# Performance work log

Hardware: AMD Instinct MI355X
Metric: run time of the kernel (lower is better)

Reference implementation:

```python
import jax, jax.numpy as jnp
import numpy as np

B, N, OBS, HID, H = 8, 1024, 64, 192, 3
D = HID // H  # head_dim = 64
ALPHA = 0.2   # LeakyReLU negative slope
NEG = -9e15   # mask value from torch code (-9000000000000000.0)


def gat_layer(h, adj, W, a):
    """Multi-head GAT layer, math-identical to the torch per-head loop.
    h: (B,N,F_in), adj: (N,N), W: (H,F_in,D), a: (H,2D).
    Concat-score a^T [Wh_i || Wh_j] is split into a_l^T Wh_i + a_r^T Wh_j
    (broadcast-add) to avoid materializing the N^2 x 2D tensor.
    """
    Wh = jnp.einsum('bni,hid->bhnd', h, W)           # (B,H,N,D)
    d = Wh.shape[-1]
    s_i = jnp.einsum('bhnd,hd->bhn', Wh, a[:, :d])   # a_l . Wh_i
    s_j = jnp.einsum('bhnd,hd->bhn', Wh, a[:, d:])   # a_r . Wh_j
    e = s_i[..., :, None] + s_j[..., None, :]        # (B,H,N,N)
    e = jnp.where(e > 0, e, ALPHA * e)               # LeakyReLU
    e = jnp.where(adj > 0, e, NEG)                   # adjacency mask
    attn = jax.nn.softmax(e, axis=-1)                # (dropout=0 in eval)
    out = jnp.einsum('bhnm,bhmd->bhnd', attn, Wh)    # weighted aggregate
    b, nh, n, _ = out.shape
    return out.transpose(0, 2, 1, 3).reshape(b, n, nh * d)  # concat heads


def setup_inputs() -> dict:
    key = jax.random.key(0)
    k1, k2, k3, k4, k5 = jax.random.split(key, 5)
    h = jax.random.normal(k1, (B, N, OBS), dtype=jnp.float32)
    adj = jnp.ones((N, N), dtype=jnp.float32)  # graph_type='full'
    # xavier_uniform-style scale (gain=1.414)
    def xav(k, shape, fan_in, fan_out):
        lim = 1.414 * np.sqrt(6.0 / (fan_in + fan_out))
        return jax.random.uniform(k, shape, jnp.float32, -lim, lim)
    W1 = xav(k2, (H, OBS, D), OBS, D)
    a1 = xav(k3, (H, 2 * D), 2 * D, 1)
    W2 = xav(k4, (H, HID, D), HID, D)
    a2 = xav(k5, (H, 2 * D), 2 * D, 1)
    return {"h": h, "adj": adj, "W1": W1, "a1": a1, "W2": W2, "a2": a2}


def reference(h, adj, W1, a1, W2, a2):
    x = gat_layer(h, adj, W1, a1)   # (B,N,HID)
    x = jax.nn.elu(x)               # inter-layer nonlinearity
    x = gat_layer(x, adj, W2, a2)   # (B,N,HID)
    return x
```

## Files before the change

### kernel.cpp

```cpp
#include <hip/hip_runtime.h>
#include <math.h>

#define Bc   8
#define Nc   1024
#define OBSc 64
#define HIDc 192
#define NHc  3
#define Dc   64
#define ALPHAc 0.2f

typedef __attribute__((ext_vector_type(8))) _Float16 half8;
typedef __attribute__((ext_vector_type(4))) float floatx4;


__global__ __launch_bounds__(256) void k_proj1(
    const float* __restrict__ xin, const float* __restrict__ W1,
    const float* __restrict__ a1, _Float16* __restrict__ WhT,
    float* __restrict__ si, float* __restrict__ sj, float* __restrict__ Mp1,
    const float* __restrict__ adj, unsigned long long* __restrict__ adjb,
    const float* __restrict__ W2, _Float16* __restrict__ W2T)
{
    const int tid = threadIdx.x;
    const int bh  = blockIdx.y;

    if (bh == Bc * NHc) {
        const int px = blockIdx.x, wv = tid >> 6, lane = tid & 63;
        for (int r8 = 0; r8 < 8; ++r8) {
            const int i = px * 32 + wv * 8 + r8;
            unsigned long long word = 0;
            for (int g = 0; g < 16; ++g) {
                bool c = adj[(size_t)i * Nc + g * 64 + lane] > 0.f;
                unsigned long long bal = __ballot(c);
                if (lane == g) word = bal;
            }
            if (lane < 16) adjb[(size_t)i * 16 + lane] = word;
        }
        if (px < 12) {
            for (int e = px * 3072 + tid; e < px * 3072 + 3072; e += 256) {
                int t = e & 7, ln = (e >> 3) & 63, p = (e >> 9) & 1, nh = (e >> 10) & 1;
                int g = e >> 11; int ks = g % 6, hh = g / 6;
                int k = ks * 32 + (ln >> 4) * 8 + t;
                int d = nh * 32 + p * 16 + (ln & 15);
                W2T[e] = (_Float16)W2[((size_t)hh * HIDc + k) * Dc + d];
            }
        }
        return;
    }

    __shared__ union {
        _Float16 Bs[64][OBSc + 8];
        _Float16 Ts[64][40];
    } u;
    __shared__ float spsAi[32], spsAj[32], spsBi[32], spsBj[32];

    const int b = bh / NHc, hh = bh % NHc;
    const int row0 = blockIdx.x * 32;

    for (int e = tid; e < OBSc * 64; e += 256) {
        int k = e >> 6, d = e & 63;
        u.Bs[d][k] = (_Float16)W1[(size_t)hh * OBSc * 64 + e];
    }
    __syncthreads();

    const int lane = tid & 63, wv = tid >> 6;
    const int mblk = (wv & 1) * 16, nhalf = (wv >> 1) * 32;
    const int fr = lane & 15, fq = lane >> 4;
    floatx4 acc0 = {0.f,0.f,0.f,0.f}, acc1 = {0.f,0.f,0.f,0.f};
    const int row = row0 + mblk + fr;

#pragma unroll
    for (int ks = 0; ks < OBSc / 32; ++ks) {
        const int k0 = ks * 32 + fq * 8;
        const float* xr = xin + ((size_t)b * Nc + row) * OBSc + k0;
        float4 u0 = *(const float4*)xr;
        float4 u1 = *(const float4*)(xr + 4);
        half8 af;
        af[0] = (_Float16)u0.x; af[1] = (_Float16)u0.y;
        af[2] = (_Float16)u0.z; af[3] = (_Float16)u0.w;
        af[4] = (_Float16)u1.x; af[5] = (_Float16)u1.y;
        af[6] = (_Float16)u1.z; af[7] = (_Float16)u1.w;
        half8 b0 = *(const half8*)&u.Bs[nhalf + fr][k0];
        half8 b1 = *(const half8*)&u.Bs[nhalf + 16 + fr][k0];
        acc0 = __builtin_amdgcn_mfma_f32_16x16x32_f16(af, b0, acc0, 0, 0, 0);
        acc1 = __builtin_amdgcn_mfma_f32_16x16x32_f16(af, b1, acc1, 0, 0, 0);
    }

    const float al0 = a1[hh * 2 * Dc + nhalf + fr];
    const float al1 = a1[hh * 2 * Dc + nhalf + 16 + fr];
    const float ar0 = a1[hh * 2 * Dc + Dc + nhalf + fr];
    const float ar1 = a1[hh * 2 * Dc + Dc + nhalf + 16 + fr];
    float pi[4], pj[4];
#pragma unroll
    for (int r = 0; r < 4; ++r) {
        pi[r] = acc0[r] * al0 + acc1[r] * al1;
        pj[r] = acc0[r] * ar0 + acc1[r] * ar1;
        for (int off = 8; off >= 1; off >>= 1) {
            pi[r] += __shfl_xor(pi[r], off, 64);
            pj[r] += __shfl_xor(pj[r], off, 64);
        }
    }
    if (fr == 0) {
#pragma unroll
        for (int r = 0; r < 4; ++r) {
            int lr = mblk + fq * 4 + r;
            if (nhalf == 0) { spsAi[lr] = pi[r]; spsAj[lr] = pj[r]; }
            else            { spsBi[lr] = pi[r]; spsBj[lr] = pj[r]; }
        }
    }
    __syncthreads();
    if (tid < 64) {
        float vj = -INFINITY;
        if (tid < 32) {
            size_t g = (size_t)bh * Nc + row0 + tid;
            si[g] = spsAi[tid] + spsBi[tid];
            vj    = spsAj[tid] + spsBj[tid];
            sj[g] = vj;
        }
        float mv = vj;
        for (int off = 32; off >= 1; off >>= 1) mv = fmaxf(mv, __shfl_xor(mv, off, 64));
        if (tid == 0) Mp1[bh * 32 + blockIdx.x] = mv;
    }

#pragma unroll
    for (int nt = 0; nt < 2; ++nt) {
        const int d = nhalf + nt * 16 + fr;
        floatx4 acc = nt ? acc1 : acc0;
#pragma unroll
        for (int p = 0; p < 2; ++p) {
            union { unsigned int w; _Float16 h[2]; } pk;
            pk.h[0] = (_Float16)acc[2 * p];
            pk.h[1] = (_Float16)acc[2 * p + 1];
            *(unsigned int*)&u.Ts[d][mblk + fq * 4 + 2 * p] = pk.w;
        }
    }
    __syncthreads();
    {
        const int c2 = tid >> 6, lane2 = tid & 63;
        const int fr2 = lane2 & 15, fq2 = lane2 >> 4;
        const int jt = row0 >> 5;
        uint4 v = *(const uint4*)&u.Ts[c2 * 16 + fr2][fq2 * 8];
        *(uint4*)&WhT[(size_t)(bh * 32 + jt) * 2048 + tid * 8] = v;
    }
}

__global__ __launch_bounds__(384, 2) void k_fused(
    const _Float16* __restrict__ WhT1,
    const float* __restrict__ si1, const float* __restrict__ sj1,
    const float* __restrict__ Mp1, const unsigned long long* __restrict__ adjb,
    const _Float16* __restrict__ W2T, const float* __restrict__ a2,
    _Float16* __restrict__ WhT2,
    float* __restrict__ si2, float* __restrict__ sj2, float* __restrict__ Mp2)
{
    __shared__ union {
        struct { float red[6][64][20]; float zs[6][16]; } ag;
        _Float16 Ts3[3][64][24];
    } uR;
    __shared__ _Float16 xhs[16][208];
    __shared__ float sp2i[6][16], sp2j[6][16];
    __shared__ float sjs[3][1024];
    __shared__ unsigned long long adjs[16][16];

    const int tid = threadIdx.x, wv = tid >> 6, lane = tid & 63;
    const int b = blockIdx.x >> 6, c16 = blockIdx.x & 63;
    const int row0 = c16 * 16;
    const int hh = wv >> 1, kh = wv & 1;
    const int bh = b * NHc + hh;
    const int fr = lane & 15, fq = lane >> 4;
    const int row = row0 + fr;

    for (int e = tid; e < 768; e += 384) {
        int h = e >> 8, idx = (e & 255) * 4;
        *(float4*)&sjs[h][idx] = *(const float4*)&sj1[(size_t)(b * NHc + h) * Nc + idx];
    }
    if (tid < 256)
        adjs[tid >> 4][tid & 15] = adjb[(size_t)(row0 + (tid >> 4)) * 16 + (tid & 15)];
    __syncthreads();

    float mpv = Mp1[bh * 32 + (lane & 31)];
    for (int off = 16; off >= 1; off >>= 1) mpv = fmaxf(mpv, __shfl_xor(mpv, off, 64));
    const float s_i = si1[(size_t)bh * Nc + row];
    const float em  = s_i + mpv;
    const float m_i = fmaxf(em, ALPHAc * em);

    const _Float16* Bp = WhT1 + (size_t)bh * 65536 + (size_t)kh * 32768 + lane * 8;

    floatx4 acc[4] = {{0.f,0.f,0.f,0.f},{0.f,0.f,0.f,0.f},
                      {0.f,0.f,0.f,0.f},{0.f,0.f,0.f,0.f}};
    float zacc = 0.f;

    half8 bf[3][4];
#pragma unroll
    for (int st = 0; st < 2; ++st)
#pragma unroll
        for (int c = 0; c < 4; ++c)
            bf[st][c] = *(const half8*)(Bp + (size_t)st * 2048 + c * 512);

#pragma unroll
    for (int s16 = 0; s16 < 16; ++s16) {
        const int s   = kh * 16 + s16;
        const int cur = s16 % 3;
        if (s16 < 14) {
            const int nxt = (s16 + 2) % 3;
            const _Float16* bn = Bp + (size_t)(s16 + 2) * 2048;
#pragma unroll
            for (int c = 0; c < 4; ++c)
                bf[nxt][c] = *(const half8*)(bn + c * 512);
        }
        const float4 sa = *(const float4*)&sjs[hh][s * 32 + fq * 8];
        const float4 sb = *(const float4*)&sjs[hh][s * 32 + fq * 8 + 4];
        const unsigned long long w = adjs[fr][s >> 1];
        const int bb = (s & 1) * 32 + fq * 8;
        const float sv[8] = {sa.x, sa.y, sa.z, sa.w, sb.x, sb.y, sb.z, sb.w};
        float p[8];
        if (w == ~0ULL) {
#pragma unroll
            for (int t = 0; t < 8; ++t) {
                float e = s_i + sv[t];
                e = fmaxf(e, ALPHAc * e) - m_i;
                p[t] = __expf(e);
            }
        } else {
#pragma unroll
            for (int t = 0; t < 8; ++t) {
                float e = s_i + sv[t];
                e = fmaxf(e, ALPHAc * e) - m_i;
                e = ((w >> (bb + t)) & 1) ? e : -1e30f;
                p[t] = __expf(e);
            }
        }
        zacc += ((p[0] + p[1]) + (p[2] + p[3])) + ((p[4] + p[5]) + (p[6] + p[7]));
        union { half8 v; _Float16 h[8]; } A;
#pragma unroll
        for (int t = 0; t < 8; ++t) A.h[t] = (_Float16)p[t];
        acc[0] = __builtin_amdgcn_mfma_f32_16x16x32_f16(A.v, bf[cur][0], acc[0], 0, 0, 0);
        acc[1] = __builtin_amdgcn_mfma_f32_16x16x32_f16(A.v, bf[cur][1], acc[1], 0, 0, 0);
        acc[2] = __builtin_amdgcn_mfma_f32_16x16x32_f16(A.v, bf[cur][2], acc[2], 0, 0, 0);
        acc[3] = __builtin_amdgcn_mfma_f32_16x16x32_f16(A.v, bf[cur][3], acc[3], 0, 0, 0);
    }

    zacc += __shfl_xor(zacc, 16, 64);
    zacc += __shfl_xor(zacc, 32, 64);
    if (lane < 16) uR.ag.zs[wv][lane] = zacc;
#pragma unroll
    for (int c = 0; c < 4; ++c)
        *(floatx4*)&uR.ag.red[wv][lane][c * 4] = acc[c];
    __syncthreads();

    {
        const int w0 = hh * 2;
#pragma unroll
        for (int cc = 0; cc < 2; ++cc) {
            const int c = kh * 2 + cc;
#pragma unroll
            for (int reg = 0; reg < 4; ++reg) {
                const int r = fq * 4 + reg;
                const float af = uR.ag.red[w0][lane][c * 4 + reg]
                               + uR.ag.red[w0 + 1][lane][c * 4 + reg];
                const float Z = uR.ag.zs[w0][r] + uR.ag.zs[w0 + 1][r];
                float v = af / Z;
                v = v > 0.f ? v : expm1f(v);
                xhs[r][hh * 64 + c * 16 + fr] = (_Float16)v;
            }
        }
    }
    __syncthreads();

    floatx4 a2c0 = {0.f,0.f,0.f,0.f}, a2c1 = {0.f,0.f,0.f,0.f};
#pragma unroll
    for (int ks = 0; ks < 6; ++ks) {
        half8 af2 = *(const half8*)&xhs[fr][ks * 32 + fq * 8];
        const _Float16* wb = W2T + (size_t)((hh * 6 + ks) * 2 + kh) * 1024 + lane * 8;
        half8 b0 = *(const half8*)wb;
        half8 b1 = *(const half8*)(wb + 512);
        a2c0 = __builtin_amdgcn_mfma_f32_16x16x32_f16(af2, b0, a2c0, 0, 0, 0);
        a2c1 = __builtin_amdgcn_mfma_f32_16x16x32_f16(af2, b1, a2c1, 0, 0, 0);
    }

    {
        const float* a2h = a2 + hh * 2 * Dc;
        const float al0 = a2h[kh * 32 + fr];
        const float al1 = a2h[kh * 32 + 16 + fr];
        const float ar0 = a2h[Dc + kh * 32 + fr];
        const float ar1 = a2h[Dc + kh * 32 + 16 + fr];
#pragma unroll
        for (int reg = 0; reg < 4; ++reg) {
            float pi = a2c0[reg] * al0 + a2c1[reg] * al1;
            float pj = a2c0[reg] * ar0 + a2c1[reg] * ar1;
            for (int off = 8; off >= 1; off >>= 1) {
                pi += __shfl_xor(pi, off, 64);
                pj += __shfl_xor(pj, off, 64);
            }
            if (fr == 0) {
                sp2i[wv][fq * 4 + reg] = pi;
                sp2j[wv][fq * 4 + reg] = pj;
            }
        }
    }
    __syncthreads();

    if (kh == 0 && lane < 16) {
        const int r = lane;
        float vi = sp2i[wv][r] + sp2i[wv + 1][r];
        float vj = sp2j[wv][r] + sp2j[wv + 1][r];
        si2[(size_t)bh * Nc + row0 + r] = vi;
        sj2[(size_t)bh * Nc + row0 + r] = vj;
        float mv = vj;
        for (int off = 8; off >= 1; off >>= 1) mv = fmaxf(mv, __shfl_xor(mv, off, 64));
        if (r == 0) Mp2[bh * 64 + c16] = mv;
    }
#pragma unroll
    for (int cc = 0; cc < 2; ++cc) {
        const int d = kh * 32 + cc * 16 + fr;
        floatx4 av = cc ? a2c1 : a2c0;
#pragma unroll
        for (int p = 0; p < 2; ++p) {
            union { unsigned int w2; _Float16 h[2]; } pk;
            pk.h[0] = (_Float16)av[2 * p];
            pk.h[1] = (_Float16)av[2 * p + 1];
            *(unsigned int*)&uR.Ts3[hh][d][fq * 4 + 2 * p] = pk.w2;
        }
    }
    __syncthreads();

    {
        const int hh3 = tid / 128, rem = tid % 128, d3 = rem >> 1, rr = rem & 1;
        uint4 v = *(const uint4*)&uR.Ts3[hh3][d3][rr * 8];
        const int bh3 = b * NHc + hh3;
        const int jt = c16 >> 1;
        const int c3 = d3 >> 4;
        const int fqp = (c16 & 1) * 2 + rr;
        *(uint4*)&WhT2[((((size_t)(bh3 * 32 + jt) * 4 + c3) * 64) + fqp * 16 + (d3 & 15)) * 8] = v;
    }
}

__global__ __launch_bounds__(256, 4) void k_aggr2(
    const _Float16* __restrict__ WhT,
    const float* __restrict__ si, const float* __restrict__ sj,
    const float* __restrict__ Mp2, const unsigned long long* __restrict__ adjb,
    float* __restrict__ out)
{
    __shared__ float red[4][64][20];
    __shared__ float zs[4][16];
    __shared__ float sjs[1024];
    __shared__ unsigned long long adjs[16][16];

    const int tid  = threadIdx.x;
    const int wv   = tid >> 6, lane = tid & 63;
    const int bh   = blockIdx.x >> 6;
    const int row0 = (blockIdx.x & 63) << 4;
    const int b    = bh / NHc, hh = bh % NHc;
    const int fr   = lane & 15, fq = lane >> 4;
    const int row  = row0 + fr;

    for (int e = tid; e < 256; e += 256)
        *(float4*)&sjs[e * 4] = *(const float4*)&sj[(size_t)bh * Nc + e * 4];
    if (tid < 256 && tid >= 0) {  }
    if (tid < 256)
        adjs[tid >> 4][tid & 15] = adjb[(size_t)(row0 + (tid >> 4)) * 16 + (tid & 15)];
    __syncthreads();

    float mpv = Mp2[bh * 64 + lane];
    for (int off = 32; off >= 1; off >>= 1) mpv = fmaxf(mpv, __shfl_xor(mpv, off, 64));

    const float s_i = si[(size_t)bh * Nc + row];
    const float em  = s_i + mpv;
    const float m_i = fmaxf(em, ALPHAc * em);

    const _Float16* Bp = WhT + (size_t)bh * 65536 + (size_t)wv * 8 * 2048 + lane * 8;

    floatx4 acc[4] = {{0.f,0.f,0.f,0.f},{0.f,0.f,0.f,0.f},
                      {0.f,0.f,0.f,0.f},{0.f,0.f,0.f,0.f}};
    float zacc = 0.f;

    half8 bf[3][4];
#pragma unroll
    for (int st = 0; st < 2; ++st)
#pragma unroll
        for (int c = 0; c < 4; ++c)
            bf[st][c] = *(const half8*)(Bp + (size_t)st * 2048 + c * 512);

#pragma unroll
    for (int s8 = 0; s8 < 8; ++s8) {
        const int s   = wv * 8 + s8;
        const int cur = s8 % 3;
        if (s8 < 6) {
            const int nxt = (s8 + 2) % 3;
            const _Float16* bn = Bp + (size_t)(s8 + 2) * 2048;
#pragma unroll
            for (int c = 0; c < 4; ++c)
                bf[nxt][c] = *(const half8*)(bn + c * 512);
        }
        const float4 sa = *(const float4*)&sjs[s * 32 + fq * 8];
        const float4 sb = *(const float4*)&sjs[s * 32 + fq * 8 + 4];
        const unsigned long long w = adjs[fr][s >> 1];
        const int bb = (s & 1) * 32 + fq * 8;
        const float sv[8] = {sa.x, sa.y, sa.z, sa.w, sb.x, sb.y, sb.z, sb.w};
        float p[8];
        if (w == ~0ULL) {
#pragma unroll
            for (int t = 0; t < 8; ++t) {
                float e = s_i + sv[t];
                e = fmaxf(e, ALPHAc * e) - m_i;
                p[t] = __expf(e);
            }
        } else {
#pragma unroll
            for (int t = 0; t < 8; ++t) {
                float e = s_i + sv[t];
                e = fmaxf(e, ALPHAc * e) - m_i;
                e = ((w >> (bb + t)) & 1) ? e : -1e30f;
                p[t] = __expf(e);
            }
        }
        zacc += ((p[0] + p[1]) + (p[2] + p[3])) + ((p[4] + p[5]) + (p[6] + p[7]));
        union { half8 v; _Float16 h[8]; } A;
#pragma unroll
        for (int t = 0; t < 8; ++t) A.h[t] = (_Float16)p[t];
        acc[0] = __builtin_amdgcn_mfma_f32_16x16x32_f16(A.v, bf[cur][0], acc[0], 0, 0, 0);
        acc[1] = __builtin_amdgcn_mfma_f32_16x16x32_f16(A.v, bf[cur][1], acc[1], 0, 0, 0);
        acc[2] = __builtin_amdgcn_mfma_f32_16x16x32_f16(A.v, bf[cur][2], acc[2], 0, 0, 0);
        acc[3] = __builtin_amdgcn_mfma_f32_16x16x32_f16(A.v, bf[cur][3], acc[3], 0, 0, 0);
    }

    zacc += __shfl_xor(zacc, 16, 64);
    zacc += __shfl_xor(zacc, 32, 64);
    if (lane < 16) zs[wv][lane] = zacc;
#pragma unroll
    for (int c = 0; c < 4; ++c)
        *(floatx4*)&red[wv][lane][c * 4] = acc[c];
    __syncthreads();

    floatx4 af = {0.f, 0.f, 0.f, 0.f};
#pragma unroll
    for (int w2 = 0; w2 < 4; ++w2) {
        floatx4 r = *(const floatx4*)&red[w2][lane][wv * 4];
        af[0] += r[0]; af[1] += r[1]; af[2] += r[2]; af[3] += r[3];
    }
#pragma unroll
    for (int reg = 0; reg < 4; ++reg) {
        const int r = fq * 4 + reg;
        const float Z = (zs[0][r] + zs[1][r]) + (zs[2][r] + zs[3][r]);
        out[((size_t)b * Nc + row0 + r) * HIDc + hh * Dc + wv * 16 + fr] = af[reg] / Z;
    }
}

extern "C" void kernel_launch(void* const* d_in, const int* in_sizes, int n_in,
                              void* d_out, int out_size, void* d_ws, size_t ws_size,
                              hipStream_t stream) {
    const float* h_in = (const float*)d_in[0];
    const float* adj  = (const float*)d_in[1];
    const float* W1   = (const float*)d_in[2];
    const float* a1   = (const float*)d_in[3];
    const float* W2   = (const float*)d_in[4];
    const float* a2   = (const float*)d_in[5];
    float* out = (float*)d_out;

    float* ws = (float*)d_ws;
    const size_t nWhT_f = (size_t)Bc * NHc * Dc * Nc / 2;
    const size_t nAb_f  = (size_t)Nc * 16 * 2;
    const size_t nW2T_f = 36864 / 2;
    const size_t nR     = (size_t)Bc * NHc * Nc;
    _Float16* WhT1 = (_Float16*)ws;
    _Float16* WhT2 = (_Float16*)(ws + nWhT_f);
    unsigned long long* adjb = (unsigned long long*)(ws + 2 * nWhT_f);
    _Float16* W2T  = (_Float16*)(ws + 2 * nWhT_f + nAb_f);
    float* si1 = ws + 2 * nWhT_f + nAb_f + nW2T_f;
    float* sj1 = si1 + nR;
    float* si2 = sj1 + nR;
    float* sj2 = si2 + nR;
    float* Mp1 = sj2 + nR;
    float* Mp2 = Mp1 + 768;

    k_proj1<<<dim3(Nc / 32, Bc * NHc + 1), 256, 0, stream>>>(
        h_in, W1, a1, WhT1, si1, sj1, Mp1, adj, adjb, W2, W2T);

    k_fused<<<512, 384, 0, stream>>>(
        WhT1, si1, sj1, Mp1, adjb, W2T, a2, WhT2, si2, sj2, Mp2);

    k_aggr2<<<1536, 256, 0, stream>>>(WhT2, si2, sj2, Mp2, adjb, out);
}
```

Measured before the change: 117.6 us.

## Enlarge row tiles to 64 and stage Wh tiles through double-buffered LDS

Both attention kernels now process 64 query rows per block instead of 16. Each block streams the full key range through double-buffered shared memory, and waves split rows instead of keys, which removes the cross-wave split-K reduction through LDS. The aim is to reuse each loaded Wh tile across more rows and cut redundant global reads. In exchange, grids shrink to 128 and 384 blocks, which lowers parallelism on a many-CU GPU, and a __syncthreads is added per key step.

Measured after the change: 127.7 us. 1.09x slower.

```diff
diff --git a/kernel.cpp b/kernel.cpp
--- a/kernel.cpp
+++ b/kernel.cpp
@@ -152,184 +152,195 @@
     float* __restrict__ si2, float* __restrict__ sj2, float* __restrict__ Mp2)
 {
     __shared__ union {
-        struct { float red[6][64][20]; float zs[6][16]; } ag;
-        _Float16 Ts3[3][64][24];
-    } uR;
-    __shared__ _Float16 xhs[16][208];
-    __shared__ float sp2i[6][16], sp2j[6][16];
+        _Float16 bufs[2][3][2048];
+        _Float16 Ts3[3][64][72];
+    } u;
+    __shared__ _Float16 xhs[64][216];
     __shared__ float sjs[3][1024];
-    __shared__ unsigned long long adjs[16][16];
+    __shared__ unsigned long long adjs[64][16];
 
     const int tid = threadIdx.x, wv = tid >> 6, lane = tid & 63;
-    const int b = blockIdx.x >> 6, c16 = blockIdx.x & 63;
-    const int row0 = c16 * 16;
-    const int hh = wv >> 1, kh = wv & 1;
+    const int b = blockIdx.x >> 4, c64 = blockIdx.x & 15;
+    const int row0 = c64 * 64;
+    const int hh = wv >> 1, mh = wv & 1;
     const int bh = b * NHc + hh;
     const int fr = lane & 15, fq = lane >> 4;
-    const int row = row0 + fr;
 
     for (int e = tid; e < 768; e += 384) {
         int h = e >> 8, idx = (e & 255) * 4;
         *(float4*)&sjs[h][idx] = *(const float4*)&sj1[(size_t)(b * NHc + h) * Nc + idx];
     }
-    if (tid < 256)
-        adjs[tid >> 4][tid & 15] = adjb[(size_t)(row0 + (tid >> 4)) * 16 + (tid & 15)];
-    __syncthreads();
+    for (int e = tid; e < 1024; e += 384)
+        adjs[e >> 4][e & 15] = adjb[(size_t)(row0 + (e >> 4)) * 16 + (e & 15)];
+
+    const int sh = tid / 128;
+    const int so = (tid & 127) * 8;
+    const _Float16* SBp = WhT1 + (size_t)(b * NHc + sh) * 65536 + so;
+    uint4 st0 = *(const uint4*)(SBp);
+    uint4 st1 = *(const uint4*)(SBp + 1024);
+    *(uint4*)&u.bufs[0][sh][so] = st0;
+    *(uint4*)&u.bufs[0][sh][so + 1024] = st1;
+    st0 = *(const uint4*)(SBp + 2048);
+    st1 = *(const uint4*)(SBp + 2048 + 1024);
 
     float mpv = Mp1[bh * 32 + (lane & 31)];
     for (int off = 16; off >= 1; off >>= 1) mpv = fmaxf(mpv, __shfl_xor(mpv, off, 64));
-    const float s_i = si1[(size_t)bh * Nc + row];
-    const float em  = s_i + mpv;
-    const float m_i = fmaxf(em, ALPHAc * em);
-
-    const _Float16* Bp = WhT1 + (size_t)bh * 65536 + (size_t)kh * 32768 + lane * 8;
-
-    floatx4 acc[4] = {{0.f,0.f,0.f,0.f},{0.f,0.f,0.f,0.f},
-                      {0.f,0.f,0.f,0.f},{0.f,0.f,0.f,0.f}};
-    float zacc = 0.f;
-
-    half8 bf[3][4];
-#pragma unroll
-    for (int st = 0; st < 2; ++st)
-#pragma unroll
-        for (int c = 0; c < 4; ++c)
-            bf[st][c] = *(const half8*)(Bp + (size_t)st * 2048 + c * 512);
-
-#pragma unroll
-    for (int s16 = 0; s16 < 16; ++s16) {
-        const int s   = kh * 16 + s16;
-        const int cur = s16 % 3;
-        if (s16 < 14) {
-            const int nxt = (s16 + 2) % 3;
-            const _Float16* bn = Bp + (size_t)(s16 + 2) * 2048;
-#pragma unroll
-            for (int c = 0; c < 4; ++c)
-                bf[nxt][c] = *(const half8*)(bn + c * 512);
+    float s_i[2], m_i[2];
+#pragma unroll
+    for (int mt = 0; mt < 2; ++mt) {
+        s_i[mt] = si1[(size_t)bh * Nc + row0 + mh * 32 + mt * 16 + fr];
+        float em = s_i[mt] + mpv;
+        m_i[mt] = fmaxf(em, ALPHAc * em);
+    }
+    __syncthreads();
+
+    floatx4 acc[2][4] = {{{0.f,0.f,0.f,0.f},{0.f,0.f,0.f,0.f},{0.f,0.f,0.f,0.f},{0.f,0.f,0.f,0.f}},
+                         {{0.f,0.f,0.f,0.f},{0.f,0.f,0.f,0.f},{0.f,0.f,0.f,0.f},{0.f,0.f,0.f,0.f}}};
+    float zacc[2] = {0.f, 0.f};
+
+#pragma unroll 2
+    for (int s = 0; s < 32; ++s) {
+        const int cur = s & 1;
+        if (s < 31) {
+            *(uint4*)&u.bufs[cur ^ 1][sh][so] = st0;
+            *(uint4*)&u.bufs[cur ^ 1][sh][so + 1024] = st1;
+            if (s < 30) {
+                st0 = *(const uint4*)(SBp + (size_t)(s + 2) * 2048);
+                st1 = *(const uint4*)(SBp + (size_t)(s + 2) * 2048 + 1024);
+            }
         }
         const float4 sa = *(const float4*)&sjs[hh][s * 32 + fq * 8];
         const float4 sb = *(const float4*)&sjs[hh][s * 32 + fq * 8 + 4];
-        const unsigned long long w = adjs[fr][s >> 1];
+        const float sv[8] = {sa.x, sa.y, sa.z, sa.w, sb.x, sb.y, sb.z, sb.w};
         const int bb = (s & 1) * 32 + fq * 8;
-        const float sv[8] = {sa.x, sa.y, sa.z, sa.w, sb.x, sb.y, sb.z, sb.w};
-        float p[8];
-        if (w == ~0ULL) {
-#pragma unroll
-            for (int t = 0; t < 8; ++t) {
-                float e = s_i + sv[t];
-                e = fmaxf(e, ALPHAc * e) - m_i;
-                p[t] = __expf(e);
-            }
-        } else {
-#pragma unroll
-            for (int t = 0; t < 8; ++t) {
-                float e = s_i + sv[t];
-                e = fmaxf(e, ALPHAc * e) - m_i;
-                e = ((w >> (bb + t)) & 1) ? e : -1e30f;
-                p[t] = __expf(e);
-            }
-        }
-        zacc += ((p[0] + p[1]) + (p[2] + p[3])) + ((p[4] + p[5]) + (p[6] + p[7]));
-        union { half8 v; _Float16 h[8]; } A;
-#pragma unroll
-        for (int t = 0; t < 8; ++t) A.h[t] = (_Float16)p[t];
-        acc[0] = __builtin_amdgcn_mfma_f32_16x16x32_f16(A.v, bf[cur][0], acc[0], 0, 0, 0);
-        acc[1] = __builtin_amdgcn_mfma_f32_16x16x32_f16(A.v, bf[cur][1], acc[1], 0, 0, 0);
-        acc[2] = __builtin_amdgcn_mfma_f32_16x16x32_f16(A.v, bf[cur][2], acc[2], 0, 0, 0);
-        acc[3] = __builtin_amdgcn_mfma_f32_16x16x32_f16(A.v, bf[cur][3], acc[3], 0, 0, 0);
-    }
-
-    zacc += __shfl_xor(zacc, 16, 64);
-    zacc += __shfl_xor(zacc, 32, 64);
-    if (lane < 16) uR.ag.zs[wv][lane] = zacc;
-#pragma unroll
-    for (int c = 0; c < 4; ++c)
-        *(floatx4*)&uR.ag.red[wv][lane][c * 4] = acc[c];
-    __syncthreads();
-
-    {
-        const int w0 = hh * 2;
-#pragma unroll
-        for (int cc = 0; cc < 2; ++cc) {
-            const int c = kh * 2 + cc;
+        half8 Av[2];
+#pragma unroll
+        for (int mt = 0; mt < 2; ++mt) {
+            const unsigned long long w = adjs[mh * 32 + mt * 16 + fr][s >> 1];
+            float p[8];
+            if (w == ~0ULL) {
+#pragma unroll
+                for (int t = 0; t < 8; ++t) {
+                    float e = s_i[mt] + sv[t];
+                    e = fmaxf(e, ALPHAc * e) - m_i[mt];
+                    p[t] = __expf(e);
+                }
+            } else {
+#pragma unroll
+                for (int t = 0; t < 8; ++t) {
+                    float e = s_i[mt] + sv[t];
+                    e = fmaxf(e, ALPHAc * e) - m_i[mt];
+                    e = ((w >> (bb + t)) & 1) ? e : -1e30f;
+                    p[t] = __expf(e);
+                }
+            }
+            zacc[mt] += ((p[0]+p[1]) + (p[2]+p[3])) + ((p[4]+p[5]) + (p[6]+p[7]));
+            union { half8 v; _Float16 h[8]; } A;
+#pragma unroll
+            for (int t = 0; t < 8; ++t) A.h[t] = (_Float16)p[t];
+            Av[mt] = A.v;
+        }
+#pragma unroll
+        for (int c = 0; c < 4; ++c) {
+            half8 bf = *(const half8*)&u.bufs[cur][hh][c * 512 + lane * 8];
+            acc[0][c] = __builtin_amdgcn_mfma_f32_16x16x32_f16(Av[0], bf, acc[0][c], 0, 0, 0);
+            acc[1][c] = __builtin_amdgcn_mfma_f32_16x16x32_f16(Av[1], bf, acc[1][c], 0, 0, 0);
+        }
+        __syncthreads();
+    }
+
+#pragma unroll
+    for (int mt = 0; mt < 2; ++mt) {
+        zacc[mt] += __shfl_xor(zacc[mt], 16, 64);
+        zacc[mt] += __shfl_xor(zacc[mt], 32, 64);
+    }
+#pragma unroll
+    for (int mt = 0; mt < 2; ++mt)
+#pragma unroll
+        for (int c = 0; c < 4; ++c)
 #pragma unroll
             for (int reg = 0; reg < 4; ++reg) {
                 const int r = fq * 4 + reg;
-                const float af = uR.ag.red[w0][lane][c * 4 + reg]
-                               + uR.ag.red[w0 + 1][lane][c * 4 + reg];
-                const float Z = uR.ag.zs[w0][r] + uR.ag.zs[w0 + 1][r];
-                float v = af / Z;
+                const float Z = __shfl(zacc[mt], r, 64);
+                float v = acc[mt][c][reg] / Z;
                 v = v > 0.f ? v : expm1f(v);
-                xhs[r][hh * 64 + c * 16 + fr] = (_Float16)v;
-            }
-        }
-    }
-    __syncthreads();
-
-    floatx4 a2c0 = {0.f,0.f,0.f,0.f}, a2c1 = {0.f,0.f,0.f,0.f};
+                xhs[mh * 32 + mt * 16 + r][hh * 64 + c * 16 + fr] = (_Float16)v;
+            }
+    __syncthreads();
+
+    floatx4 acc2[2][4] = {{{0.f,0.f,0.f,0.f},{0.f,0.f,0.f,0.f},{0.f,0.f,0.f,0.f},{0.f,0.f,0.f,0.f}},
+                          {{0.f,0.f,0.f,0.f},{0.f,0.f,0.f,0.f},{0.f,0.f,0.f,0.f},{0.f,0.f,0.f,0.f}}};
 #pragma unroll
     for (int ks = 0; ks < 6; ++ks) {
-        half8 af2 = *(const half8*)&xhs[fr][ks * 32 + fq * 8];
-        const _Float16* wb = W2T + (size_t)((hh * 6 + ks) * 2 + kh) * 1024 + lane * 8;
-        half8 b0 = *(const half8*)wb;
-        half8 b1 = *(const half8*)(wb + 512);
-        a2c0 = __builtin_amdgcn_mfma_f32_16x16x32_f16(af2, b0, a2c0, 0, 0, 0);
-        a2c1 = __builtin_amdgcn_mfma_f32_16x16x32_f16(af2, b1, a2c1, 0, 0, 0);
-    }
-
-    {
-        const float* a2h = a2 + hh * 2 * Dc;
-        const float al0 = a2h[kh * 32 + fr];
-        const float al1 = a2h[kh * 32 + 16 + fr];
-        const float ar0 = a2h[Dc + kh * 32 + fr];
-        const float ar1 = a2h[Dc + kh * 32 + 16 + fr];
+        half8 a0 = *(const half8*)&xhs[mh * 32 + fr][ks * 32 + fq * 8];
+        half8 a1 = *(const half8*)&xhs[mh * 32 + 16 + fr][ks * 32 + fq * 8];
+#pragma unroll
+        for (int nh = 0; nh < 2; ++nh) {
+            const _Float16* wb = W2T + (size_t)((hh * 6 + ks) * 2 + nh) * 1024 + lane * 8;
+            half8 b0 = *(const half8*)wb;
+            half8 b1 = *(const half8*)(wb + 512);
+            acc2[0][nh*2+0] = __builtin_amdgcn_mfma_f32_16x16x32_f16(a0, b0, acc2[0][nh*2+0], 0, 0, 0);
+            acc2[0][nh*2+1] = __builtin_amdgcn_mfma_f32_16x16x32_f16(a0, b1, acc2[0][nh*2+1], 0, 0, 0);
+            acc2[1][nh*2+0] = __builtin_amdgcn_mfma_f32_16x16x32_f16(a1, b0, acc2[1][nh*2+0], 0, 0, 0);
+            acc2[1][nh*2+1] = __builtin_amdgcn_mfma_f32_16x16x32_f16(a1, b1, acc2[1][nh*2+1], 0, 0, 0);
+        }
+    }
+
+    const float* a2h = a2 + hh * 2 * Dc;
+    float maxpj = -INFINITY;
+#pragma unroll
+    for (int mt = 0; mt < 2; ++mt)
 #pragma unroll
         for (int reg = 0; reg < 4; ++reg) {
-            float pi = a2c0[reg] * al0 + a2c1[reg] * al1;
-            float pj = a2c0[reg] * ar0 + a2c1[reg] * ar1;
+            float pi = 0.f, pj = 0.f;
+#pragma unroll
+            for (int nh = 0; nh < 2; ++nh)
+#pragma unroll
+                for (int p = 0; p < 2; ++p) {
+                    const int d = nh * 32 + p * 16 + fr;
+                    pi += acc2[mt][nh*2+p][reg] * a2h[d];
+                    pj += acc2[mt][nh*2+p][reg] * a2h[Dc + d];
+                }
             for (int off = 8; off >= 1; off >>= 1) {
                 pi += __shfl_xor(pi, off, 64);
                 pj += __shfl_xor(pj, off, 64);
             }
             if (fr == 0) {
-                sp2i[wv][fq * 4 + reg] = pi;
-                sp2j[wv][fq * 4 + reg] = pj;
-            }
-        }
-    }
-    __syncthreads();
-
-    if (kh == 0 && lane < 16) {
-        const int r = lane;
-        float vi = sp2i[wv][r] + sp2i[wv + 1][r];
-        float vj = sp2j[wv][r] + sp2j[wv + 1][r];
-        si2[(size_t)bh * Nc + row0 + r] = vi;
-        sj2[(size_t)bh * Nc + row0 + r] = vj;
-        float mv = vj;
-        for (int off = 8; off >= 1; off >>= 1) mv = fmaxf(mv, __shfl_xor(mv, off, 64));
-        if (r == 0) Mp2[bh * 64 + c16] = mv;
-    }
-#pragma unroll
-    for (int cc = 0; cc < 2; ++cc) {
-        const int d = kh * 32 + cc * 16 + fr;
-        floatx4 av = cc ? a2c1 : a2c0;
-#pragma unroll
-        for (int p = 0; p < 2; ++p) {
-            union { unsigned int w2; _Float16 h[2]; } pk;
-            pk.h[0] = (_Float16)av[2 * p];
-            pk.h[1] = (_Float16)av[2 * p + 1];
-            *(unsigned int*)&uR.Ts3[hh][d][fq * 4 + 2 * p] = pk.w2;
-        }
-    }
-    __syncthreads();
-
-    {
-        const int hh3 = tid / 128, rem = tid % 128, d3 = rem >> 1, rr = rem & 1;
-        uint4 v = *(const uint4*)&uR.Ts3[hh3][d3][rr * 8];
-        const int bh3 = b * NHc + hh3;
-        const int jt = c16 >> 1;
-        const int c3 = d3 >> 4;
-        const int fqp = (c16 & 1) * 2 + rr;
-        *(uint4*)&WhT2[((((size_t)(bh3 * 32 + jt) * 4 + c3) * 64) + fqp * 16 + (d3 & 15)) * 8] = v;
+                const size_t g = (size_t)bh * Nc + row0 + mh * 32 + mt * 16 + fq * 4 + reg;
+                si2[g] = pi;
+                sj2[g] = pj;
+            }
+            maxpj = fmaxf(maxpj, pj);
+        }
+    maxpj = fmaxf(maxpj, __shfl_xor(maxpj, 16, 64));
+    maxpj = fmaxf(maxpj, __shfl_xor(maxpj, 32, 64));
+    if (lane == 0) Mp2[bh * 32 + c64 * 2 + mh] = maxpj;
+
+#pragma unroll
+    for (int mt = 0; mt < 2; ++mt)
+#pragma unroll
+        for (int nh = 0; nh < 2; ++nh)
+#pragma unroll
+            for (int p = 0; p < 2; ++p) {
+                const int d = nh * 32 + p * 16 + fr;
+#pragma unroll
+                for (int pp = 0; pp < 2; ++pp) {
+                    union { unsigned int w2; _Float16 h[2]; } pk;
+                    pk.h[0] = (_Float16)acc2[mt][nh*2+p][2*pp];
+                    pk.h[1] = (_Float16)acc2[mt][nh*2+p][2*pp+1];
+                    *(unsigned int*)&u.Ts3[hh][d][mh*32 + mt*16 + fq*4 + 2*pp] = pk.w2;
+                }
+            }
+    __syncthreads();
+
+#pragma unroll
+    for (int q = 0; q < 4; ++q) {
+        const int e = q * 384 + tid;
+        const int ehh = e >> 9, rem = e & 511;
+        const int jt = rem >> 8, rem2 = rem & 255;
+        const int c = rem2 >> 6, ln = rem2 & 63;
+        uint4 v = *(const uint4*)&u.Ts3[ehh][c * 16 + (ln & 15)][jt * 32 + (ln >> 4) * 8];
+        *(uint4*)&WhT2[((size_t)((b * NHc + ehh) * 32 + (c64 * 2 + jt)) * 2048) + (c * 64 + ln) * 8] = v;
     }
 }
 
@@ -339,60 +350,49 @@
     const float* __restrict__ Mp2, const unsigned long long* __restrict__ adjb,
     float* __restrict__ out)
 {
-    __shared__ float red[4][64][20];
-    __shared__ float zs[4][16];
+    __shared__ _Float16 bufs[2][2048];
     __shared__ float sjs[1024];
-    __shared__ unsigned long long adjs[16][16];
-
-    const int tid  = threadIdx.x;
-    const int wv   = tid >> 6, lane = tid & 63;
-    const int bh   = blockIdx.x >> 6;
-    const int row0 = (blockIdx.x & 63) << 4;
-    const int b    = bh / NHc, hh = bh % NHc;
-    const int fr   = lane & 15, fq = lane >> 4;
-    const int row  = row0 + fr;
-
-    for (int e = tid; e < 256; e += 256)
-        *(float4*)&sjs[e * 4] = *(const float4*)&sj[(size_t)bh * Nc + e * 4];
-    if (tid < 256 && tid >= 0) {  }
-    if (tid < 256)
-        adjs[tid >> 4][tid & 15] = adjb[(size_t)(row0 + (tid >> 4)) * 16 + (tid & 15)];
-    __syncthreads();
-
-    float mpv = Mp2[bh * 64 + lane];
-    for (int off = 32; off >= 1; off >>= 1) mpv = fmaxf(mpv, __shfl_xor(mpv, off, 64));
-
+    __shared__ unsigned long long adjs[64][16];
+
+    const int tid = threadIdx.x, wv = tid >> 6, lane = tid & 63;
+    const int bh = blockIdx.x >> 4;
+    const int row0 = (blockIdx.x & 15) << 6;
+    const int b = bh / NHc, hh = bh % NHc;
+    const int fr = lane & 15, fq = lane >> 4;
+    const int rl = wv * 16 + fr;
+    const int row = row0 + rl;
+
+    *(float4*)&sjs[tid * 4] = *(const float4*)&sj[(size_t)bh * Nc + tid * 4];
+    for (int e = tid; e < 1024; e += 256)
+        adjs[e >> 4][e & 15] = adjb[(size_t)(row0 + (e >> 4)) * 16 + (e & 15)];
+
+    float mpv = Mp2[bh * 32 + (lane & 31)];
+    for (int off = 16; off >= 1; off >>= 1) mpv = fmaxf(mpv, __shfl_xor(mpv, off, 64));
     const float s_i = si[(size_t)bh * Nc + row];
     const float em  = s_i + mpv;
     const float m_i = fmaxf(em, ALPHAc * em);
 
-    const _Float16* Bp = WhT + (size_t)bh * 65536 + (size_t)wv * 8 * 2048 + lane * 8;
+    const int so = tid * 8;
+    const _Float16* SBp = WhT + (size_t)bh * 65536 + so;
+    uint4 st = *(const uint4*)(SBp);
+    *(uint4*)&bufs[0][so] = st;
+    st = *(const uint4*)(SBp + 2048);
+    __syncthreads();
 
     floatx4 acc[4] = {{0.f,0.f,0.f,0.f},{0.f,0.f,0.f,0.f},
                       {0.f,0.f,0.f,0.f},{0.f,0.f,0.f,0.f}};
     float zacc = 0.f;
 
-    half8 bf[3][4];
-#pragma unroll
-    for (int st = 0; st < 2; ++st)
-#pragma unroll
-        for (int c = 0; c < 4; ++c)
-            bf[st][c] = *(const half8*)(Bp + (size_t)st * 2048 + c * 512);
-
-#pragma unroll
-    for (int s8 = 0; s8 < 8; ++s8) {
-        const int s   = wv * 8 + s8;
-        const int cur = s8 % 3;
-        if (s8 < 6) {
-            const int nxt = (s8 + 2) % 3;
-            const _Float16* bn = Bp + (size_t)(s8 + 2) * 2048;
-#pragma unroll
-            for (int c = 0; c < 4; ++c)
-                bf[nxt][c] = *(const half8*)(bn + c * 512);
+#pragma unroll 2
+    for (int s = 0; s < 32; ++s) {
+        const int cur = s & 1;
+        if (s < 31) {
+            *(uint4*)&bufs[cur ^ 1][so] = st;
+            if (s < 30) st = *(const uint4*)(SBp + (size_t)(s + 2) * 2048);
         }
         const float4 sa = *(const float4*)&sjs[s * 32 + fq * 8];
         const float4 sb = *(const float4*)&sjs[s * 32 + fq * 8 + 4];
-        const unsigned long long w = adjs[fr][s >> 1];
+        const unsigned long long w = adjs[rl][s >> 1];
         const int bb = (s & 1) * 32 + fq * 8;
         const float sv[8] = {sa.x, sa.y, sa.z, sa.w, sb.x, sb.y, sb.z, sb.w};
         float p[8];
@@ -412,36 +412,29 @@
                 p[t] = __expf(e);
             }
         }
-        zacc += ((p[0] + p[1]) + (p[2] + p[3])) + ((p[4] + p[5]) + (p[6] + p[7]));
+        zacc += ((p[0]+p[1]) + (p[2]+p[3])) + ((p[4]+p[5]) + (p[6]+p[7]));
         union { half8 v; _Float16 h[8]; } A;
 #pragma unroll
         for (int t = 0; t < 8; ++t) A.h[t] = (_Float16)p[t];
-        acc[0] = __builtin_amdgcn_mfma_f32_16x16x32_f16(A.v, bf[cur][0], acc[0], 0, 0, 0);
-        acc[1] = __builtin_amdgcn_mfma_f32_16x16x32_f16(A.v, bf[cur][1], acc[1], 0, 0, 0);
-        acc[2] = __builtin_amdgcn_mfma_f32_16x16x32_f16(A.v, bf[cur][2], acc[2], 0, 0, 0);
-        acc[3] = __builtin_amdgcn_mfma_f32_16x16x32_f16(A.v, bf[cur][3], acc[3], 0, 0, 0);
+#pragma unroll
+        for (int c = 0; c < 4; ++c) {
+            half8 bf = *(const half8*)&bufs[cur][c * 512 + lane * 8];
+            acc[c] = __builtin_amdgcn_mfma_f32_16x16x32_f16(A.v, bf, acc[c], 0, 0, 0);
+        }
+        __syncthreads();
     }
 
     zacc += __shfl_xor(zacc, 16, 64);
     zacc += __shfl_xor(zacc, 32, 64);
-    if (lane < 16) zs[wv][lane] = zacc;
 #pragma unroll
     for (int c = 0; c < 4; ++c)
-        *(floatx4*)&red[wv][lane][c * 4] = acc[c];
-    __syncthreads();
-
-    floatx4 af = {0.f, 0.f, 0.f, 0.f};
-#pragma unroll
-    for (int w2 = 0; w2 < 4; ++w2) {
-        floatx4 r = *(const floatx4*)&red[w2][lane][wv * 4];
-        af[0] += r[0]; af[1] += r[1]; af[2] += r[2]; af[3] += r[3];
-    }
-#pragma unroll
-    for (int reg = 0; reg < 4; ++reg) {
-        const int r = fq * 4 + reg;
-        const float Z = (zs[0][r] + zs[1][r]) + (zs[2][r] + zs[3][r]);
-        out[((size_t)b * Nc + row0 + r) * HIDc + hh * Dc + wv * 16 + fr] = af[reg] / Z;
-    }
+#pragma unroll
+        for (int reg = 0; reg < 4; ++reg) {
+            const int r = fq * 4 + reg;
+            const float Z = __shfl(zacc, r, 64);
+            out[((size_t)b * Nc + row0 + wv * 16 + r) * HIDc + hh * Dc + c * 16 + fr]
+                = acc[c][reg] / Z;
+        }
 }
 
 extern "C" void kernel_launch(void* const* d_in, const int* in_sizes, int n_in,
@@ -474,8 +467,8 @@
     k_proj1<<<dim3(Nc / 32, Bc * NHc + 1), 256, 0, stream>>>(
         h_in, W1, a1, WhT1, si1, sj1, Mp1, adj, adjb, W2, W2T);
 
-    k_fused<<<512, 384, 0, stream>>>(
+    k_fused<<<128, 384, 0, stream>>>(
         WhT1, si1, sj1, Mp1, adjb, W2T, a2, WhT2, si2, sj2, Mp2);
 
-    k_aggr2<<<1536, 256, 0, stream>>>(WhT2, si2, sj2, Mp2, adjb, out);
+    k_aggr2<<<384, 256, 0, stream>>>(WhT2, si2, sj2, Mp2, adjb, out);
 }
```
